# Kernel tuning notes

Hardware: AMD Instinct MI355X
Metric: run time of the kernel (lower is better)

The kernel has to match this reference:

```python
import jax, jax.numpy as jnp
import numpy as np

IN, OUT, EDGE_FEAT = 32, 32, 16
B, N = 8, 128            # batch, nodes per graph; E = B*N*N edges
H1, H2, H3 = 128, 256, 128  # NNet hidden sizes (nmp_qc default)


def _linear_params(key, n_in, n_out):
    kw, kb = jax.random.split(key)
    s = 1.0 / np.sqrt(n_in)
    W = jax.random.uniform(kw, (n_in, n_out), jnp.float32, -s, s)
    b = jax.random.uniform(kb, (n_out,), jnp.float32, -s, s)
    return W, b


def setup_inputs() -> dict:
    key = jax.random.key(0)
    ks = jax.random.split(key, 8)
    h_v = jax.random.normal(ks[0], (B, N, IN), jnp.float32)
    h_w = jax.random.normal(ks[1], (B * N, IN), jnp.float32)
    e_vw = jax.random.normal(ks[2], (B * N * N, EDGE_FEAT), jnp.float32)
    W1, b1 = _linear_params(ks[3], EDGE_FEAT, H1)
    W2, b2 = _linear_params(ks[4], H1, H2)
    W3, b3 = _linear_params(ks[5], H2, H3)
    W4, b4 = _linear_params(ks[6], H3, IN * OUT)
    return {"h_v": h_v, "h_w": h_w, "e_vw": e_vw,
            "W1": W1, "b1": b1, "W2": W2, "b2": b2,
            "W3": W3, "b3": b3, "W4": W4, "b4": b4}


def reference(h_v, h_w, e_vw, W1, b1, W2, b2, W3, b3, W4, b4):
    # Edge-conditioned weight generator (NNet MLP with ReLU hidden layers)
    x = jax.nn.relu(e_vw @ W1 + b1)
    x = jax.nn.relu(x @ W2 + b2)
    x = jax.nn.relu(x @ W3 + b3)
    edge_output = x @ W4 + b4                      # (E, out*in)
    edge_output = edge_output.reshape(-1, OUT, IN)  # (E, out, in)

    # h_w_rows: expand h_w (B*N, in) with a trailing dim of size h_v.size(1)=N,
    # then flatten to rows of length `in` (exact replica of the torch view).
    n_v = h_v.shape[1]
    h_w_rows = jnp.broadcast_to(h_w[:, :, None],
                                (h_w.shape[0], h_w.shape[1], n_v))
    h_w_rows = h_w_rows.reshape(-1, IN)            # (E, in)

    # bmm of per-edge (out, in) matrix with (in,) vector, then squeeze
    m_new = jnp.einsum('eoi,ei->eo', edge_output, h_w_rows)  # (E, out)
    return m_new
```

## Files before the change

kernel.cpp:

```cpp
#include <hip/hip_runtime.h>


typedef _Float16 f16;
typedef _Float16 f16x8 __attribute__((ext_vector_type(8)));
typedef __fp16 fp16x2 __attribute__((ext_vector_type(2)));
typedef float f32x4 __attribute__((ext_vector_type(4)));

#define OFF_W1S 0
#define OFF_W2S 4096
#define OFF_W3S 36864
#define OFF_W4S 69632
#define WS_HALFS 73728

union U16x8 { struct { uint2 lo, hi; } p; f16x8 v; };
union U32x2 { fp16x2 h2[2]; uint2 u; };

__global__ void prep_kernel(const float* __restrict__ W1, const float* __restrict__ b1,
                            const float* __restrict__ W2, const float* __restrict__ W3,
                            const float* __restrict__ W4, const float* __restrict__ b4,
                            f16* __restrict__ wsh, float* __restrict__ b4r) {
  int t = blockIdx.x * 256 + threadIdx.x;
  if (t < 4096) {
    int j = t & 7, l = (t >> 3) & 63, ct = t >> 9;
    int k = ((l >> 4) & 3) * 8 + j, c = ct * 16 + (l & 15);
    wsh[OFF_W1S + t] = (k < 16) ? (f16)W1[k * 128 + c]
                                : (k == 16 ? (f16)b1[c] : (f16)0.f);
  } else if (t < 36864) {
    int s = t - 4096;
    int j = s & 7, l = (s >> 3) & 63, kt = (s >> 9) & 3, ct = s >> 11;
    int k = kt * 32 + ((l >> 4) & 3) * 8 + j, c = ct * 16 + (l & 15);
    wsh[t] = (f16)W2[k * 256 + c];
  } else if (t < 69632) {
    int s = t - 36864;
    int j = s & 7, l = (s >> 3) & 63, kt = (s >> 9) & 7, ct = s >> 12;
    int k = kt * 32 + ((l >> 4) & 3) * 8 + j, c = ct * 16 + (l & 15);
    wsh[t] = (f16)W3[k * 128 + c];
  } else if (t < 73728) {
    int s = t - 69632;
    int j = s & 7, l = (s >> 3) & 63, kt = (s >> 9) & 3, ct = s >> 11;
    int k = kt * 32 + ((l >> 4) & 3) * 8 + j, o = ct * 16 + (l & 15);
    float a = 0.f;
#pragma unroll
    for (int i = 0; i < 32; ++i) a += W4[k * 1024 + o * 32 + i];
    wsh[t] = (f16)a;
  }
  if (t < 32) {
    float a = 0.f;
#pragma unroll
    for (int i = 0; i < 32; ++i) a += b4[t * 32 + i];
    b4r[t] = a;
  }
}

__global__ __launch_bounds__(256, 3) void mlp_mfma_kernel(
    const float* __restrict__ e_vw, const float* __restrict__ h_w,
    const float* __restrict__ b2, const float* __restrict__ b3,
    const f16* __restrict__ wsh, const float* __restrict__ b4r,
    float* __restrict__ out) {
  __shared__ f16 P[64 * 132];
  __shared__ f16 Q[64 * 260];

  const int l  = threadIdx.x & 63;
  const int w  = threadIdx.x >> 6;
  const int e0 = l & 15;
  const int kg = l >> 4;
  const size_t row0 = (size_t)blockIdx.x * 64;

  {
    int rl = threadIdx.x >> 2;
    int c4 = (threadIdx.x & 3) * 4;
    float4 v = *reinterpret_cast<const float4*>(e_vw + (row0 + rl) * 16 + c4);
    union { f16 h[4]; uint2 u; } pk;
    pk.h[0] = (f16)v.x; pk.h[1] = (f16)v.y; pk.h[2] = (f16)v.z; pk.h[3] = (f16)v.w;
    *reinterpret_cast<uint2*>(Q + rl * 36 + c4) = pk.u;
    union { f16 h[4]; uint2 u; } z;
    z.h[0] = (c4 == 0) ? (f16)1.f : (f16)0.f; z.h[1] = (f16)0.f;
    z.h[2] = (f16)0.f; z.h[3] = (f16)0.f;
    *reinterpret_cast<uint2*>(Q + rl * 36 + 16 + c4) = z.u;
  }

  const f16x8* wp1 = (const f16x8*)(wsh + OFF_W1S);
  f16x8 bfr1[2];
#pragma unroll
  for (int c = 0; c < 2; ++c) bfr1[c] = wp1[(2 * w + c) * 64 + l];
  __syncthreads();

  {
#pragma unroll
    for (int t = 0; t < 4; ++t) {
      const f16* pa = Q + (t * 16 + e0) * 36 + kg * 8;
      U16x8 a; a.p.lo = *(const uint2*)pa; a.p.hi = *(const uint2*)(pa + 4);
#pragma unroll
      for (int c = 0; c < 2; ++c) {
        f32x4 acc = {0.f, 0.f, 0.f, 0.f};
        acc = __builtin_amdgcn_mfma_f32_16x16x32_f16(bfr1[c], a.v, acc, 0, 0, 0);
        U32x2 o;
        o.h2[0] = __builtin_amdgcn_cvt_pkrtz(fmaxf(acc[0], 0.f), fmaxf(acc[1], 0.f));
        o.h2[1] = __builtin_amdgcn_cvt_pkrtz(fmaxf(acc[2], 0.f), fmaxf(acc[3], 0.f));
        *reinterpret_cast<uint2*>(P + (t * 16 + e0) * 132 + (2 * w + c) * 16 + kg * 4) = o.u;
      }
    }
  }
  const f16x8* wp2 = (const f16x8*)(wsh + OFF_W2S);
  f16x8 bfr2[16];
#pragma unroll
  for (int c = 0; c < 4; ++c)
#pragma unroll
    for (int kt = 0; kt < 4; ++kt)
      bfr2[c * 4 + kt] = wp2[((4 * w + c) * 4 + kt) * 64 + l];
  __syncthreads();

  {
    float4 bb[4];
#pragma unroll
    for (int c = 0; c < 4; ++c)
      bb[c] = *reinterpret_cast<const float4*>(b2 + (4 * w + c) * 16 + kg * 4);
#pragma unroll
    for (int t = 0; t < 4; ++t) {
      const f16* pa = P + (t * 16 + e0) * 132 + kg * 8;
      U16x8 a[4];
#pragma unroll
      for (int kt = 0; kt < 4; ++kt) {
        a[kt].p.lo = *(const uint2*)(pa + kt * 32);
        a[kt].p.hi = *(const uint2*)(pa + kt * 32 + 4);
      }
#pragma unroll
      for (int c = 0; c < 4; ++c) {
        f32x4 acc = {0.f, 0.f, 0.f, 0.f};
#pragma unroll
        for (int kt = 0; kt < 4; ++kt)
          acc = __builtin_amdgcn_mfma_f32_16x16x32_f16(bfr2[c * 4 + kt], a[kt].v, acc, 0, 0, 0);
        U32x2 o;
        o.h2[0] = __builtin_amdgcn_cvt_pkrtz(fmaxf(acc[0] + bb[c].x, 0.f),
                                             fmaxf(acc[1] + bb[c].y, 0.f));
        o.h2[1] = __builtin_amdgcn_cvt_pkrtz(fmaxf(acc[2] + bb[c].z, 0.f),
                                             fmaxf(acc[3] + bb[c].w, 0.f));
        *reinterpret_cast<uint2*>(Q + (t * 16 + e0) * 260 + (4 * w + c) * 16 + kg * 4) = o.u;
      }
    }
  }
  const f16x8* wp3 = (const f16x8*)(wsh + OFF_W3S);
  f16x8 bfr3[16];
#pragma unroll
  for (int c = 0; c < 2; ++c)
#pragma unroll
    for (int kt = 0; kt < 8; ++kt)
      bfr3[c * 8 + kt] = wp3[((2 * w + c) * 8 + kt) * 64 + l];
  __syncthreads();

  {
    float4 bb[2];
#pragma unroll
    for (int c = 0; c < 2; ++c)
      bb[c] = *reinterpret_cast<const float4*>(b3 + (2 * w + c) * 16 + kg * 4);
#pragma unroll
    for (int t = 0; t < 4; ++t) {
      const f16* pa = Q + (t * 16 + e0) * 260 + kg * 8;
      U16x8 a[8];
#pragma unroll
      for (int kt = 0; kt < 8; ++kt) {
        a[kt].p.lo = *(const uint2*)(pa + kt * 32);
        a[kt].p.hi = *(const uint2*)(pa + kt * 32 + 4);
      }
#pragma unroll
      for (int c = 0; c < 2; ++c) {
        f32x4 acc = {0.f, 0.f, 0.f, 0.f};
#pragma unroll
        for (int kt = 0; kt < 8; ++kt)
          acc = __builtin_amdgcn_mfma_f32_16x16x32_f16(bfr3[c * 8 + kt], a[kt].v, acc, 0, 0, 0);
        U32x2 o;
        o.h2[0] = __builtin_amdgcn_cvt_pkrtz(fmaxf(acc[0] + bb[c].x, 0.f),
                                             fmaxf(acc[1] + bb[c].y, 0.f));
        o.h2[1] = __builtin_amdgcn_cvt_pkrtz(fmaxf(acc[2] + bb[c].z, 0.f),
                                             fmaxf(acc[3] + bb[c].w, 0.f));
        *reinterpret_cast<uint2*>(P + (t * 16 + e0) * 132 + (2 * w + c) * 16 + kg * 4) = o.u;
      }
    }
  }
  const f16x8* wp4 = (const f16x8*)(wsh + OFF_W4S);
  const int ct = w & 1;
  const int tb = (w >> 1) * 2;
  f16x8 bfr4[4];
#pragma unroll
  for (int kt = 0; kt < 4; ++kt) bfr4[kt] = wp4[(ct * 4 + kt) * 64 + l];
  __syncthreads();

  {
    float4 bb = *reinterpret_cast<const float4*>(b4r + ct * 16 + kg * 4);
#pragma unroll
    for (int ti = 0; ti < 2; ++ti) {
      int t = tb + ti;
      const f16* pa = P + (t * 16 + e0) * 132 + kg * 8;
      U16x8 a[4];
#pragma unroll
      for (int kt = 0; kt < 4; ++kt) {
        a[kt].p.lo = *(const uint2*)(pa + kt * 32);
        a[kt].p.hi = *(const uint2*)(pa + kt * 32 + 4);
      }
      f32x4 acc = {0.f, 0.f, 0.f, 0.f};
#pragma unroll
      for (int kt = 0; kt < 4; ++kt)
        acc = __builtin_amdgcn_mfma_f32_16x16x32_f16(bfr4[kt], a[kt].v, acc, 0, 0, 0);
      size_t e = row0 + t * 16 + e0;
      float s = h_w[(e >> 7) * 32 + ((e & 127) >> 2)];
      float4 st;
      st.x = s * (acc[0] + bb.x); st.y = s * (acc[1] + bb.y);
      st.z = s * (acc[2] + bb.z); st.w = s * (acc[3] + bb.w);
      *reinterpret_cast<float4*>(out + e * 32 + ct * 16 + kg * 4) = st;
    }
  }
}

extern "C" void kernel_launch(void* const* d_in, const int* in_sizes, int n_in,
                              void* d_out, int out_size, void* d_ws, size_t ws_size,
                              hipStream_t stream) {
  const float* h_w  = (const float*)d_in[1];
  const float* e_vw = (const float*)d_in[2];
  const float* W1   = (const float*)d_in[3];
  const float* b1   = (const float*)d_in[4];
  const float* W2   = (const float*)d_in[5];
  const float* b2   = (const float*)d_in[6];
  const float* W3   = (const float*)d_in[7];
  const float* b3   = (const float*)d_in[8];
  const float* W4   = (const float*)d_in[9];
  const float* b4   = (const float*)d_in[10];
  float* out = (float*)d_out;

  f16*   wsh = (f16*)d_ws;
  float* b4r = (float*)((char*)d_ws + (size_t)WS_HALFS * 2);

  const int E = in_sizes[2] / 16;

  hipLaunchKernelGGL(prep_kernel, dim3(288), dim3(256), 0, stream,
                     W1, b1, W2, W3, W4, b4, wsh, b4r);
  hipLaunchKernelGGL(mlp_mfma_kernel, dim3(E / 64), dim3(256), 0, stream,
                     e_vw, h_w, b2, b3, wsh, b4r, out);
}
```

Before: 32.63 us.

## Split layer-2/3 MLP into K-halves to shrink LDS and registers, raise occupancy

Layer 2's 256 outputs are computed in two halves of 128 columns. Each half is fed straight into a partial layer-3 accumulation held in registers, so the 64x256 intermediate buffer is replaced by two 64x128 buffers. This cuts LDS per block and the per-wave weight fragment registers, and the launch bound rises from 3 to 4 blocks per SIMD. Layer 1 now reads e_vw directly from global memory into MFMA operands, which removes the staging LDS write and one barrier. In exchange there are more __syncthreads and a second pass of weight loads.

```diff
diff --git a/kernel.cpp b/kernel.cpp
--- a/kernel.cpp
+++ b/kernel.cpp
@@ -52,13 +52,13 @@
   }
 }
 
-__global__ __launch_bounds__(256, 3) void mlp_mfma_kernel(
+__global__ __launch_bounds__(256, 4) void mlp_mfma_kernel(
     const float* __restrict__ e_vw, const float* __restrict__ h_w,
     const float* __restrict__ b2, const float* __restrict__ b3,
     const f16* __restrict__ wsh, const float* __restrict__ b4r,
     float* __restrict__ out) {
-  __shared__ f16 P[64 * 132];
-  __shared__ f16 Q[64 * 260];
+  __shared__ f16 B1[64 * 132];
+  __shared__ f16 B2[64 * 132];
 
   const int l  = threadIdx.x & 63;
   const int w  = threadIdx.x >> 6;
@@ -66,58 +66,64 @@
   const int kg = l >> 4;
   const size_t row0 = (size_t)blockIdx.x * 64;
 
+  const f16x8* wp1 = (const f16x8*)(wsh + OFF_W1S);
+  const f16x8* wp2 = (const f16x8*)(wsh + OFF_W2S);
+  const f16x8* wp3 = (const f16x8*)(wsh + OFF_W3S);
+  const f16x8* wp4 = (const f16x8*)(wsh + OFF_W4S);
+
+  f16x8 bfr1[2];
+#pragma unroll
+  for (int c = 0; c < 2; ++c) bfr1[c] = wp1[(2 * w + c) * 64 + l];
+
+#pragma unroll
+  for (int t = 0; t < 4; ++t) {
+    U16x8 a;
+    if (kg < 2) {
+      const float* pe = e_vw + (row0 + t * 16 + e0) * 16 + kg * 8;
+      float4 v0 = *reinterpret_cast<const float4*>(pe);
+      float4 v1 = *reinterpret_cast<const float4*>(pe + 4);
+      U32x2 c0, c1;
+      c0.h2[0] = __builtin_amdgcn_cvt_pkrtz(v0.x, v0.y);
+      c0.h2[1] = __builtin_amdgcn_cvt_pkrtz(v0.z, v0.w);
+      c1.h2[0] = __builtin_amdgcn_cvt_pkrtz(v1.x, v1.y);
+      c1.h2[1] = __builtin_amdgcn_cvt_pkrtz(v1.z, v1.w);
+      a.p.lo = c0.u; a.p.hi = c1.u;
+    } else {
+      a.p.lo.x = (kg == 2) ? 0x00003C00u : 0u;
+      a.p.lo.y = 0u; a.p.hi.x = 0u; a.p.hi.y = 0u;
+    }
+#pragma unroll
+    for (int c = 0; c < 2; ++c) {
+      f32x4 acc = {0.f, 0.f, 0.f, 0.f};
+      acc = __builtin_amdgcn_mfma_f32_16x16x32_f16(bfr1[c], a.v, acc, 0, 0, 0);
+      U32x2 o;
+      o.h2[0] = __builtin_amdgcn_cvt_pkrtz(fmaxf(acc[0], 0.f), fmaxf(acc[1], 0.f));
+      o.h2[1] = __builtin_amdgcn_cvt_pkrtz(fmaxf(acc[2], 0.f), fmaxf(acc[3], 0.f));
+      *reinterpret_cast<uint2*>(B1 + (t * 16 + e0) * 132 + (2 * w + c) * 16 + kg * 4) = o.u;
+    }
+  }
+  f16x8 bfa[8];
+#pragma unroll
+  for (int c = 0; c < 2; ++c)
+#pragma unroll
+    for (int kt = 0; kt < 4; ++kt)
+      bfa[c * 4 + kt] = wp2[((2 * w + c) * 4 + kt) * 64 + l];
+  __syncthreads();
+
+  f16x8 bfb[8];
+#pragma unroll
+  for (int c = 0; c < 2; ++c)
+#pragma unroll
+    for (int kt = 0; kt < 4; ++kt)
+      bfb[c * 4 + kt] = wp3[((2 * w + c) * 8 + kt) * 64 + l];
   {
-    int rl = threadIdx.x >> 2;
-    int c4 = (threadIdx.x & 3) * 4;
-    float4 v = *reinterpret_cast<const float4*>(e_vw + (row0 + rl) * 16 + c4);
-    union { f16 h[4]; uint2 u; } pk;
-    pk.h[0] = (f16)v.x; pk.h[1] = (f16)v.y; pk.h[2] = (f16)v.z; pk.h[3] = (f16)v.w;
-    *reinterpret_cast<uint2*>(Q + rl * 36 + c4) = pk.u;
-    union { f16 h[4]; uint2 u; } z;
-    z.h[0] = (c4 == 0) ? (f16)1.f : (f16)0.f; z.h[1] = (f16)0.f;
-    z.h[2] = (f16)0.f; z.h[3] = (f16)0.f;
-    *reinterpret_cast<uint2*>(Q + rl * 36 + 16 + c4) = z.u;
-  }
-
-  const f16x8* wp1 = (const f16x8*)(wsh + OFF_W1S);
-  f16x8 bfr1[2];
-#pragma unroll
-  for (int c = 0; c < 2; ++c) bfr1[c] = wp1[(2 * w + c) * 64 + l];
-  __syncthreads();
-
-  {
+    float4 bb[2];
+#pragma unroll
+    for (int c = 0; c < 2; ++c)
+      bb[c] = *reinterpret_cast<const float4*>(b2 + (2 * w + c) * 16 + kg * 4);
 #pragma unroll
     for (int t = 0; t < 4; ++t) {
-      const f16* pa = Q + (t * 16 + e0) * 36 + kg * 8;
-      U16x8 a; a.p.lo = *(const uint2*)pa; a.p.hi = *(const uint2*)(pa + 4);
-#pragma unroll
-      for (int c = 0; c < 2; ++c) {
-        f32x4 acc = {0.f, 0.f, 0.f, 0.f};
-        acc = __builtin_amdgcn_mfma_f32_16x16x32_f16(bfr1[c], a.v, acc, 0, 0, 0);
-        U32x2 o;
-        o.h2[0] = __builtin_amdgcn_cvt_pkrtz(fmaxf(acc[0], 0.f), fmaxf(acc[1], 0.f));
-        o.h2[1] = __builtin_amdgcn_cvt_pkrtz(fmaxf(acc[2], 0.f), fmaxf(acc[3], 0.f));
-        *reinterpret_cast<uint2*>(P + (t * 16 + e0) * 132 + (2 * w + c) * 16 + kg * 4) = o.u;
-      }
-    }
-  }
-  const f16x8* wp2 = (const f16x8*)(wsh + OFF_W2S);
-  f16x8 bfr2[16];
-#pragma unroll
-  for (int c = 0; c < 4; ++c)
-#pragma unroll
-    for (int kt = 0; kt < 4; ++kt)
-      bfr2[c * 4 + kt] = wp2[((4 * w + c) * 4 + kt) * 64 + l];
-  __syncthreads();
-
-  {
-    float4 bb[4];
-#pragma unroll
-    for (int c = 0; c < 4; ++c)
-      bb[c] = *reinterpret_cast<const float4*>(b2 + (4 * w + c) * 16 + kg * 4);
-#pragma unroll
-    for (int t = 0; t < 4; ++t) {
-      const f16* pa = P + (t * 16 + e0) * 132 + kg * 8;
+      const f16* pa = B1 + (t * 16 + e0) * 132 + kg * 8;
       U16x8 a[4];
 #pragma unroll
       for (int kt = 0; kt < 4; ++kt) {
@@ -125,40 +131,60 @@
         a[kt].p.hi = *(const uint2*)(pa + kt * 32 + 4);
       }
 #pragma unroll
-      for (int c = 0; c < 4; ++c) {
+      for (int c = 0; c < 2; ++c) {
         f32x4 acc = {0.f, 0.f, 0.f, 0.f};
 #pragma unroll
         for (int kt = 0; kt < 4; ++kt)
-          acc = __builtin_amdgcn_mfma_f32_16x16x32_f16(bfr2[c * 4 + kt], a[kt].v, acc, 0, 0, 0);
+          acc = __builtin_amdgcn_mfma_f32_16x16x32_f16(bfa[c * 4 + kt], a[kt].v, acc, 0, 0, 0);
         U32x2 o;
         o.h2[0] = __builtin_amdgcn_cvt_pkrtz(fmaxf(acc[0] + bb[c].x, 0.f),
                                              fmaxf(acc[1] + bb[c].y, 0.f));
         o.h2[1] = __builtin_amdgcn_cvt_pkrtz(fmaxf(acc[2] + bb[c].z, 0.f),
                                              fmaxf(acc[3] + bb[c].w, 0.f));
-        *reinterpret_cast<uint2*>(Q + (t * 16 + e0) * 260 + (4 * w + c) * 16 + kg * 4) = o.u;
-      }
-    }
-  }
-  const f16x8* wp3 = (const f16x8*)(wsh + OFF_W3S);
-  f16x8 bfr3[16];
+        *reinterpret_cast<uint2*>(B2 + (t * 16 + e0) * 132 + (2 * w + c) * 16 + kg * 4) = o.u;
+      }
+    }
+  }
+  __syncthreads();
+
+  f32x4 acc3[4][2];
+#pragma unroll
+  for (int t = 0; t < 4; ++t)
+#pragma unroll
+    for (int c = 0; c < 2; ++c) acc3[t][c] = (f32x4){0.f, 0.f, 0.f, 0.f};
+#pragma unroll
+  for (int t = 0; t < 4; ++t) {
+    const f16* pa = B2 + (t * 16 + e0) * 132 + kg * 8;
+    U16x8 a[4];
+#pragma unroll
+    for (int kt = 0; kt < 4; ++kt) {
+      a[kt].p.lo = *(const uint2*)(pa + kt * 32);
+      a[kt].p.hi = *(const uint2*)(pa + kt * 32 + 4);
+    }
+#pragma unroll
+    for (int c = 0; c < 2; ++c)
+#pragma unroll
+      for (int kt = 0; kt < 4; ++kt)
+        acc3[t][c] = __builtin_amdgcn_mfma_f32_16x16x32_f16(bfb[c * 4 + kt], a[kt].v, acc3[t][c], 0, 0, 0);
+  }
+  __syncthreads();
+
 #pragma unroll
   for (int c = 0; c < 2; ++c)
 #pragma unroll
-    for (int kt = 0; kt < 8; ++kt)
-      bfr3[c * 8 + kt] = wp3[((2 * w + c) * 8 + kt) * 64 + l];
-  __syncthreads();
-
+    for (int kt = 0; kt < 4; ++kt)
+      bfa[c * 4 + kt] = wp2[((8 + 2 * w + c) * 4 + kt) * 64 + l];
   {
     float4 bb[2];
 #pragma unroll
     for (int c = 0; c < 2; ++c)
-      bb[c] = *reinterpret_cast<const float4*>(b3 + (2 * w + c) * 16 + kg * 4);
+      bb[c] = *reinterpret_cast<const float4*>(b2 + (8 + 2 * w + c) * 16 + kg * 4);
 #pragma unroll
     for (int t = 0; t < 4; ++t) {
-      const f16* pa = Q + (t * 16 + e0) * 260 + kg * 8;
-      U16x8 a[8];
-#pragma unroll
-      for (int kt = 0; kt < 8; ++kt) {
+      const f16* pa = B1 + (t * 16 + e0) * 132 + kg * 8;
+      U16x8 a[4];
+#pragma unroll
+      for (int kt = 0; kt < 4; ++kt) {
         a[kt].p.lo = *(const uint2*)(pa + kt * 32);
         a[kt].p.hi = *(const uint2*)(pa + kt * 32 + 4);
       }
@@ -166,31 +192,69 @@
       for (int c = 0; c < 2; ++c) {
         f32x4 acc = {0.f, 0.f, 0.f, 0.f};
 #pragma unroll
-        for (int kt = 0; kt < 8; ++kt)
-          acc = __builtin_amdgcn_mfma_f32_16x16x32_f16(bfr3[c * 8 + kt], a[kt].v, acc, 0, 0, 0);
+        for (int kt = 0; kt < 4; ++kt)
+          acc = __builtin_amdgcn_mfma_f32_16x16x32_f16(bfa[c * 4 + kt], a[kt].v, acc, 0, 0, 0);
         U32x2 o;
         o.h2[0] = __builtin_amdgcn_cvt_pkrtz(fmaxf(acc[0] + bb[c].x, 0.f),
                                              fmaxf(acc[1] + bb[c].y, 0.f));
         o.h2[1] = __builtin_amdgcn_cvt_pkrtz(fmaxf(acc[2] + bb[c].z, 0.f),
                                              fmaxf(acc[3] + bb[c].w, 0.f));
-        *reinterpret_cast<uint2*>(P + (t * 16 + e0) * 132 + (2 * w + c) * 16 + kg * 4) = o.u;
-      }
-    }
-  }
-  const f16x8* wp4 = (const f16x8*)(wsh + OFF_W4S);
-  const int ct = w & 1;
-  const int tb = (w >> 1) * 2;
-  f16x8 bfr4[4];
-#pragma unroll
-  for (int kt = 0; kt < 4; ++kt) bfr4[kt] = wp4[(ct * 4 + kt) * 64 + l];
-  __syncthreads();
-
+        *reinterpret_cast<uint2*>(B2 + (t * 16 + e0) * 132 + (2 * w + c) * 16 + kg * 4) = o.u;
+      }
+    }
+  }
+  __syncthreads();
+
+#pragma unroll
+  for (int c = 0; c < 2; ++c)
+#pragma unroll
+    for (int kt = 0; kt < 4; ++kt)
+      bfb[c * 4 + kt] = wp3[((2 * w + c) * 8 + 4 + kt) * 64 + l];
+#pragma unroll
+  for (int t = 0; t < 4; ++t) {
+    const f16* pa = B2 + (t * 16 + e0) * 132 + kg * 8;
+    U16x8 a[4];
+#pragma unroll
+    for (int kt = 0; kt < 4; ++kt) {
+      a[kt].p.lo = *(const uint2*)(pa + kt * 32);
+      a[kt].p.hi = *(const uint2*)(pa + kt * 32 + 4);
+    }
+#pragma unroll
+    for (int c = 0; c < 2; ++c)
+#pragma unroll
+      for (int kt = 0; kt < 4; ++kt)
+        acc3[t][c] = __builtin_amdgcn_mfma_f32_16x16x32_f16(bfb[c * 4 + kt], a[kt].v, acc3[t][c], 0, 0, 0);
+  }
   {
+    float4 bb[2];
+#pragma unroll
+    for (int c = 0; c < 2; ++c)
+      bb[c] = *reinterpret_cast<const float4*>(b3 + (2 * w + c) * 16 + kg * 4);
+#pragma unroll
+    for (int t = 0; t < 4; ++t)
+#pragma unroll
+      for (int c = 0; c < 2; ++c) {
+        U32x2 o;
+        o.h2[0] = __builtin_amdgcn_cvt_pkrtz(fmaxf(acc3[t][c][0] + bb[c].x, 0.f),
+                                             fmaxf(acc3[t][c][1] + bb[c].y, 0.f));
+        o.h2[1] = __builtin_amdgcn_cvt_pkrtz(fmaxf(acc3[t][c][2] + bb[c].z, 0.f),
+                                             fmaxf(acc3[t][c][3] + bb[c].w, 0.f));
+        *reinterpret_cast<uint2*>(B1 + (t * 16 + e0) * 132 + (2 * w + c) * 16 + kg * 4) = o.u;
+      }
+  }
+  __syncthreads();
+
+  {
+    const int ct = w & 1;
+    const int tb = (w >> 1) * 2;
+    f16x8 bfr4[4];
+#pragma unroll
+    for (int kt = 0; kt < 4; ++kt) bfr4[kt] = wp4[(ct * 4 + kt) * 64 + l];
     float4 bb = *reinterpret_cast<const float4*>(b4r + ct * 16 + kg * 4);
 #pragma unroll
     for (int ti = 0; ti < 2; ++ti) {
       int t = tb + ti;
-      const f16* pa = P + (t * 16 + e0) * 132 + kg * 8;
+      const f16* pa = B1 + (t * 16 + e0) * 132 + kg * 8;
       U16x8 a[4];
 #pragma unroll
       for (int kt = 0; kt < 4; ++kt) {
```

New measurement: 39.85 us. +22.1%, slower.
